# Performance work log

Measured on AMD Instinct MI355X. Metric: run time of the kernel, lower is better.

## Reference

```python
import jax, jax.numpy as jnp
import numpy as np
from jax import lax

# Production-scale RPN detection-head config
B, FH, FW, NA = 8, 200, 200, 9      # batch, fmap h, fmap w, anchors/cell
H, W = 800, 800                      # image dims
N = FH * FW * NA                     # 360k anchors per image
NMS_THR = 0.7
MIN_SIZE = 1e-3


def _make_anchors():
    scales = np.array([32.0, 64.0, 128.0])
    ratios = np.array([0.5, 1.0, 2.0])
    ws = (scales[:, None] * np.sqrt(1.0 / ratios)[None, :]).reshape(-1)  # [NA]
    hs = (scales[:, None] * np.sqrt(ratios)[None, :]).reshape(-1)
    sy, sx = H / FH, W / FW
    cx = (np.arange(FW) + 0.5) * sx
    cy = (np.arange(FH) + 0.5) * sy
    cxg, cyg = np.meshgrid(cx, cy)                     # [FH,FW]
    cxg = cxg[..., None]; cyg = cyg[..., None]         # [FH,FW,1]
    a = np.stack([cxg - ws / 2, cyg - hs / 2, cxg + ws / 2, cyg + hs / 2], axis=-1)
    return jnp.asarray(a.reshape(-1, 4), jnp.float32)  # [N,4] xyxy


def setup_inputs() -> dict:
    key = jax.random.key(0)
    k1, k2 = jax.random.split(key)
    cls_logits = jax.random.normal(k1, (B, N, 1), jnp.float32)
    reg_deltas = jax.random.normal(k2, (B, N, 4), jnp.float32) * 0.1  # sane exp(dw)
    anchors = jnp.broadcast_to(_make_anchors()[None], (B, N, 4))
    return {
        "cls_logits": cls_logits,
        "reg_deltas": reg_deltas,
        "anchors": anchors,
        "keep_pre_nms": 1000,
        "keep_post_nms": 300,
    }


def _offsets2boxes(deltas, anchors):
    aw = anchors[:, 2] - anchors[:, 0]
    ah = anchors[:, 3] - anchors[:, 1]
    acx = anchors[:, 0] + 0.5 * aw
    acy = anchors[:, 1] + 0.5 * ah
    cx = deltas[:, 0] * aw + acx
    cy = deltas[:, 1] * ah + acy
    w = jnp.exp(deltas[:, 2]) * aw
    h = jnp.exp(deltas[:, 3]) * ah
    return jnp.stack([cx - 0.5 * w, cy - 0.5 * h, cx + 0.5 * w, cy + 0.5 * h], axis=-1)


def _iou_matrix(b):
    area = (b[:, 2] - b[:, 0]) * (b[:, 3] - b[:, 1])
    lt = jnp.maximum(b[:, None, :2], b[None, :, :2])
    rb = jnp.minimum(b[:, None, 2:], b[None, :, 2:])
    wh = jnp.clip(rb - lt, 0.0)
    inter = wh[..., 0] * wh[..., 1]
    return inter / (area[:, None] + area[None, :] - inter + 1e-9)


def _detect_one(logit, delta, anc, pre, post):
    scores = jax.nn.sigmoid(logit.reshape(-1))             # [N]
    boxes = _offsets2boxes(delta.reshape(-1, 4), anc)      # [N,4]
    s, idx = lax.top_k(scores, pre)                        # sorted desc
    b = boxes[idx]                                         # [pre,4]
    # clip to image
    b = jnp.stack([
        jnp.clip(b[:, 0], 0.0, W), jnp.clip(b[:, 1], 0.0, H),
        jnp.clip(b[:, 2], 0.0, W), jnp.clip(b[:, 3], 0.0, H)], axis=-1)
    valid = ((b[:, 2] - b[:, 0]) >= MIN_SIZE) & ((b[:, 3] - b[:, 1]) >= MIN_SIZE)
    # greedy NMS on score-sorted boxes (mask-based, fixed shapes)
    iou = _iou_matrix(lax.stop_gradient(b))                # [pre,pre]
    j = jnp.arange(pre)

    def body(keep, i):
        sup = (iou[i] > NMS_THR) & (j > i) & keep[i]
        return keep & ~sup, None

    keep, _ = lax.scan(body, valid, jnp.arange(pre))
    # compact first `post` kept detections into fixed [post,5], zero-padded
    dets = jnp.concatenate([b, s[:, None]], axis=-1)       # [pre,5]
    rank = jnp.cumsum(keep) - 1
    tgt = jnp.where(keep & (rank < post), rank, post)
    out = jnp.zeros((post + 1, 5), dets.dtype).at[tgt].set(dets)[:post]
    return out


def reference(cls_logits, reg_deltas, anchors, keep_pre_nms, keep_post_nms):
    f = lambda l, d, a: _detect_one(l, d, a, keep_pre_nms, keep_post_nms)
    return jax.vmap(f)(cls_logits, reg_deltas, anchors)    # [B,post,5]
```

## Files before the change

### kernel.cpp

```cpp
#include <hip/hip_runtime.h>
#include <stdint.h>
#include <math.h>

typedef unsigned long long u64;
typedef unsigned int u32;
typedef unsigned short u16;

#define NPI   360000
#define B_IMG 8
#define PRE   1000
#define POST  300
#define CAP   4096
#define NMSF  0.7f
#define IMG_W 800.0f
#define IMG_H 800.0f

#define NBIN    4096
#define KSHIFT  20
#define CHUNK_H 24
#define F4PB_H  (NPI / 4 / CHUNK_H)
#define CHUNK_C 48
#define F4PB_C  (NPI / 4 / CHUNK_C)
#define EPB_C   (NPI / CHUNK_C)
#define LBUF    1024

#define CNT_OFF    0
#define VALID_OFF  128
#define THRESH_OFF 2048
#define RHIST_OFF  4096
#define BHIST_OFF  135168
#define CAND_OFF   1708032
#define BOX_OFF    1970176
#define SCORE_OFF  2098176
#define MASK_OFF   2130176

__device__ __forceinline__ u32 fkey(float f) {
  u32 u = __float_as_uint(f);
  return (u & 0x80000000u) ? ~u : (u | 0x80000000u);
}
__device__ __forceinline__ u64 rl64(u64 v, int lane) {
  u32 lo = (u32)__builtin_amdgcn_readlane((int)(u32)v, lane);
  u32 hi = (u32)__builtin_amdgcn_readlane((int)(u32)(v >> 32), lane);
  return ((u64)hi << 32) | lo;
}
__device__ __forceinline__ u64 sx64(u64 v, int m) {
  u32 lo = (u32)__shfl_xor((int)(u32)v, m, 64);
  u32 hi = (u32)__shfl_xor((int)(u32)(v >> 32), m, 64);
  return ((u64)hi << 32) | lo;
}

__global__ __launch_bounds__(256) void k_hist(const float* __restrict__ logits,
                                              u32* __restrict__ bhist) {
  __shared__ u32 h[NBIN];
  const int img = blockIdx.y, c = blockIdx.x;
  for (int i = threadIdx.x; i < NBIN; i += 256) h[i] = 0;
  __syncthreads();
  const float4* L = (const float4*)(logits + (size_t)img * NPI) + (size_t)c * F4PB_H;
  for (int i = threadIdx.x; i < F4PB_H; i += 256) {
    float4 v = L[i];
    atomicAdd(&h[fkey(v.x) >> KSHIFT], 1u);
    atomicAdd(&h[fkey(v.y) >> KSHIFT], 1u);
    atomicAdd(&h[fkey(v.z) >> KSHIFT], 1u);
    atomicAdd(&h[fkey(v.w) >> KSHIFT], 1u);
  }
  __syncthreads();
  u32* O = bhist + (size_t)(img * CHUNK_H + c) * (NBIN / 2);
  for (int i = threadIdx.x; i < NBIN / 2; i += 256)
    O[i] = (h[2 * i] & 0xFFFFu) | (h[2 * i + 1] << 16);
}

__global__ __launch_bounds__(256) void k_hreduce(const u32* __restrict__ bhist,
                                                 u32* __restrict__ rhist,
                                                 u32* __restrict__ cnt,
                                                 u64* __restrict__ validw) {
  int gid = blockIdx.x * 256 + threadIdx.x;
  int img = gid >> 11, p = gid & 2047;
  u32 slo = 0, shi = 0;
#pragma unroll
  for (int c = 0; c < CHUNK_H; c++) {
    u32 v = bhist[(size_t)(img * CHUNK_H + c) * (NBIN / 2) + p];
    slo += v & 0xFFFFu;
    shi += v >> 16;
  }
  ((uint2*)rhist)[img * (NBIN / 2) + p] = make_uint2(slo, shi);
  if (blockIdx.x == 0) {
    if (threadIdx.x < 8) cnt[threadIdx.x] = 0;
    if (threadIdx.x < 128) validw[threadIdx.x] = 0ull;
  }
}

__global__ void k_select(const u32* __restrict__ hist, int* __restrict__ thresh) {
  const int img = blockIdx.x;
  const u32* H = hist + img * NBIN;
  __shared__ u32 part[256];
  u32 s = 0;
#pragma unroll
  for (int b = 0; b < 16; b++) s += H[threadIdx.x * 16 + b];
  part[threadIdx.x] = s;
  __syncthreads();
  if (threadIdx.x == 0) {
    u32 cum = 0;
    int pb = 255;
    for (; pb > 0; pb--) {
      if (cum + part[pb] >= (u32)PRE) break;
      cum += part[pb];
    }
    int bin;
    for (bin = pb * 16 + 15; bin >= pb * 16; bin--) {
      cum += H[bin];
      if (cum >= (u32)PRE) break;
    }
    if (bin < pb * 16) bin = pb * 16;
    thresh[img] = bin;
  }
}

__global__ __launch_bounds__(256) void k_compact(const float* __restrict__ logits,
                                                 const int* __restrict__ thresh,
                                                 u32* __restrict__ cnt,
                                                 u64* __restrict__ cand) {
  __shared__ u64 buf[LBUF];
  __shared__ u32 bcnt;
  __shared__ u32 gbase;
  const int img = blockIdx.y, c = blockIdx.x;
  const int tb  = thresh[img];
  if (threadIdx.x == 0) bcnt = 0;
  __syncthreads();
  const float4* L = (const float4*)(logits + (size_t)img * NPI) + (size_t)c * F4PB_C;
  const int ebase = c * EPB_C;
  for (int i = threadIdx.x; i < F4PB_C; i += 256) {
    float4 v = L[i];
    float xs[4] = {v.x, v.y, v.z, v.w};
#pragma unroll
    for (int q = 0; q < 4; q++) {
      float x = xs[q];
      if ((int)(fkey(x) >> KSHIFT) >= tb) {
        float ef = (float)exp(-(double)x);
        float sg = 1.0f / (1.0f + ef);
        u32 e = (u32)(ebase + 4 * i + q);
        u32 p = atomicAdd(&bcnt, 1u);
        if (p < LBUF)
          buf[p] = ((u64)fkey(sg) << 32) | (u64)(0xFFFFFFFFu - e);
      }
    }
  }
  __syncthreads();
  if (threadIdx.x == 0) {
    u32 m = bcnt < LBUF ? bcnt : LBUF;
    bcnt = m;
    gbase = atomicAdd(&cnt[img], m);
  }
  __syncthreads();
  const u32 m = bcnt, gb = gbase;
  for (u32 j = threadIdx.x; j < m; j += 256) {
    u32 pos = gb + j;
    if (pos < CAP) cand[img * CAP + pos] = buf[j];
  }
}

#define RB 8
__device__ __forceinline__ void emit_row(
    int img, int row, u64 key,
    const float* __restrict__ deltas, const float* __restrict__ anchors,
    float4* __restrict__ boxes, float* __restrict__ scores, u64* __restrict__ validw) {
  u32 hi  = (u32)(key >> 32);
  u32 idx = 0xFFFFFFFFu - (u32)(key & 0xFFFFFFFFu);
  u32 su  = (hi & 0x80000000u) ? (hi ^ 0x80000000u) : ~hi;
  float sc = __uint_as_float(su);
  size_t off = (size_t)img * NPI + idx;
  float4 d = ((const float4*)deltas)[off];
  float4 a = ((const float4*)anchors)[off];
  float aw = a.z - a.x, ah = a.w - a.y;
  float acx = a.x + 0.5f * aw, acy = a.y + 0.5f * ah;
  float cx = d.x * aw + acx, cy = d.y * ah + acy;
  float w = expf(d.z) * aw, h = expf(d.w) * ah;
  float x1 = cx - 0.5f * w, y1 = cy - 0.5f * h;
  float x2 = cx + 0.5f * w, y2 = cy + 0.5f * h;
  x1 = fminf(fmaxf(x1, 0.f), IMG_W);
  y1 = fminf(fmaxf(y1, 0.f), IMG_H);
  x2 = fminf(fmaxf(x2, 0.f), IMG_W);
  y2 = fminf(fmaxf(y2, 0.f), IMG_H);
  boxes[img * PRE + row]  = make_float4(x1, y1, x2, y2);
  scores[img * PRE + row] = sc;
  if (((x2 - x1) >= 1e-3f) && ((y2 - y1) >= 1e-3f))
    atomicOr(&validw[img * 16 + (row >> 6)], 1ull << (row & 63));
}

__global__ __launch_bounds__(256) void k_rank(
    const float* __restrict__ deltas, const float* __restrict__ anchors,
    const u32* __restrict__ cnt, const u64* __restrict__ cand,
    float4* __restrict__ boxes, float* __restrict__ scores, u64* __restrict__ validw) {
  __shared__ u64 skey[CAP];
  const int img = blockIdx.y;
  int n = (int)cnt[img];
  if (n > CAP) n = CAP;
  for (int i = threadIdx.x; i < n; i += 256) skey[i] = cand[img * CAP + i];
  __syncthreads();
  const int r0 = blockIdx.x * 256 + threadIdx.x;
  const int r1 = r0 + RB * 256;
  u64 k0 = (r0 < n) ? skey[r0] : 0ull;
  u64 k1 = (r1 < n) ? skey[r1] : 0ull;
  int c0 = 0, c1 = 0;
  for (int j = 0; j < n; j++) {
    u64 kj = skey[j];
    c0 += (kj > k0);
    c1 += (kj > k1);
  }
  if (r0 < n && c0 < PRE) emit_row(img, c0, k0, deltas, anchors, boxes, scores, validw);
  if (r1 < n && c1 < PRE) emit_row(img, c1, k1, deltas, anchors, boxes, scores, validw);
}

__global__ __launch_bounds__(1024) void k_iou(const float4* __restrict__ boxes,
                                              u64* __restrict__ mask) {
  __shared__ float4 sb[1024];
  __shared__ float  sa[1024];
  const int img = blockIdx.y;
  const int tid = threadIdx.x;
  {
    float4 b = (tid < PRE) ? boxes[img * PRE + tid]
                           : make_float4(0.f, 0.f, 0.f, 0.f);
    sb[tid] = b;
    sa[tid] = (b.z - b.x) * (b.w - b.y);
  }
  __syncthreads();
  const int lane = tid & 63;
  const int wv   = tid >> 6;
  const int i    = blockIdx.x * 64 + lane;
  const bool rowok = (i < PRE);
  const float4 bi = sb[blockIdx.x * 64 + lane];
  const float  ai = sa[blockIdx.x * 64 + lane];
  const int cbase = wv << 6;
  u64 bits = 0;
#pragma unroll
  for (int k = 0; k < 64; k++) {
    int c = cbase + k;
    float4 bc = sb[c];
    float ac  = sa[c];
    float ltx = fmaxf(bi.x, bc.x), lty = fmaxf(bi.y, bc.y);
    float rbx = fminf(bi.z, bc.z), rby = fminf(bi.w, bc.w);
    float iw = fmaxf(rbx - ltx, 0.f), ih = fmaxf(rby - lty, 0.f);
    float inter = iw * ih;
    float iou = inter / (ai + ac - inter + 1e-9f);
    bits |= (iou > NMSF) ? (1ull << k) : 0ull;
  }
  int d = i - cbase;
  u64 gtmask = (d < 0) ? ~0ull : ((d >= 63) ? 0ull : (~0ull << (d + 1)));
  int rem = PRE - cbase;
  u64 tmask = (rem >= 64) ? ~0ull : ((rem <= 0) ? 0ull : ((1ull << rem) - 1ull));
  bits &= gtmask & tmask;
  if (rowok) mask[((size_t)img * PRE + i) * 16 + wv] = bits;
}

#define LDSROWS 496
#define NMS_T   320
__global__ __launch_bounds__(NMS_T) void k_nms(
    const u64* __restrict__ mask, const u64* __restrict__ validw,
    const float4* __restrict__ boxes, const float* __restrict__ scores,
    float* __restrict__ out) {
  __shared__ u64 smask[LDSROWS * 16];
  __shared__ int skeeplist[POST];
  __shared__ int skept;
  const int img = blockIdx.x;
  const int tid = threadIdx.x;
  const u64* M = mask + (size_t)img * PRE * 16;
  u64 diag[16];
  if (tid < 64) {
#pragma unroll
    for (int cc = 0; cc < 16; cc++) {
      int row = cc * 64 + tid;
      diag[cc] = (row < PRE) ? M[(size_t)row * 16 + cc] : 0ull;
    }
  }
  for (int e = tid; e < LDSROWS * 16; e += NMS_T) smask[e] = M[e];
  __syncthreads();
  if (tid < 64) {
    const int lane = tid;
    const int w = lane & 15, g = lane >> 4;
    u64 rem = ~0ull;
    if (lane < 16) {
      rem = ~validw[img * 16 + lane];
      if (lane == 15) rem |= 0xFFFFFF0000000000ull;
    }
    int kept = 0;
#pragma unroll
    for (int cc = 0; cc < 16; cc++) {
      u64 alive = ~rl64(rem, cc);
      int kept0 = kept;
      while (alive != 0ull && kept < POST) {
        int r = __builtin_ctzll(alive);
        if (lane == 0) skeeplist[kept] = cc * 64 + r;
        kept++;
        u64 sup = rl64(diag[cc], r);
        alive &= ~sup;
        alive &= ~(1ull << r);
      }
      int nc = kept - kept0;
      if (nc > 0 && kept < POST && cc < 15) {
        u64 part = 0;
        for (int j = g; j < nc; j += 4) {
          int row = skeeplist[kept0 + j];
          part |= (row < LDSROWS) ? smask[row * 16 + w] : M[(size_t)row * 16 + w];
        }
        part |= sx64(part, 16);
        part |= sx64(part, 32);
        rem |= part;
      }
      if (kept >= POST) break;
    }
    if (lane == 0) skept = kept;
  }
  __syncthreads();
  if (tid < POST) {
    float4 bx = make_float4(0.f, 0.f, 0.f, 0.f);
    float  sc = 0.f;
    if (tid < skept) {
      int i = skeeplist[tid];
      bx = boxes[img * PRE + i];
      sc = scores[img * PRE + i];
    }
    float* o = out + ((size_t)img * POST + tid) * 5;
    o[0] = bx.x; o[1] = bx.y; o[2] = bx.z; o[3] = bx.w; o[4] = sc;
  }
}

extern "C" void kernel_launch(void* const* d_in, const int* in_sizes, int n_in,
                              void* d_out, int out_size, void* d_ws, size_t ws_size,
                              hipStream_t stream) {
  const float* logits  = (const float*)d_in[0];
  const float* deltas  = (const float*)d_in[1];
  const float* anchors = (const float*)d_in[2];
  float* out = (float*)d_out;
  char* ws = (char*)d_ws;

  u32* cnt      = (u32*)(ws + CNT_OFF);
  u64* validw   = (u64*)(ws + VALID_OFF);
  int* thresh   = (int*)(ws + THRESH_OFF);
  u32* rhist    = (u32*)(ws + RHIST_OFF);
  u32* bhist    = (u32*)(ws + BHIST_OFF);
  u64* cand     = (u64*)(ws + CAND_OFF);
  float4* boxes = (float4*)(ws + BOX_OFF);
  float* scores = (float*)(ws + SCORE_OFF);
  u64* mask     = (u64*)(ws + MASK_OFF);

  dim3 gh(CHUNK_H, B_IMG);
  k_hist<<<gh, 256, 0, stream>>>(logits, bhist);
  k_hreduce<<<(B_IMG * NBIN / 2) / 256, 256, 0, stream>>>(bhist, rhist, cnt, validw);
  k_select<<<B_IMG, 256, 0, stream>>>(rhist, thresh);
  dim3 gc(CHUNK_C, B_IMG);
  k_compact<<<gc, 256, 0, stream>>>(logits, thresh, cnt, cand);
  dim3 gr(RB, B_IMG);
  k_rank<<<gr, 256, 0, stream>>>(deltas, anchors, cnt, cand, boxes, scores, validw);
  dim3 g2(16, B_IMG);
  k_iou<<<g2, 1024, 0, stream>>>(boxes, mask);
  k_nms<<<B_IMG, NMS_T, 0, stream>>>(mask, validw, boxes, scores, out);
}
```

Measured before the change: 214.2 us.

## Fuse rank, IoU and NMS into one per-image kernel; merge threshold select

Replaces the separate rank, IoU-mask and NMS kernels with a single 1024-thread block per image. Boxes, areas, scores and the valid bits stay in shared memory instead of round-tripping through global workspace. The histogram reduce and threshold-select kernels become one kernel that uses a wave-level suffix scan, and the histogram moves to 8192 bins over 36 chunks. This removes several launches and intermediate global traffic, but the rank and IoU work now runs on only 8 blocks instead of many. The NMS mask reads also lose their shared-memory staging and go to global memory.

```diff
diff --git a/kernel.cpp b/kernel.cpp
--- a/kernel.cpp
+++ b/kernel.cpp
@@ -4,7 +4,6 @@
 
 typedef unsigned long long u64;
 typedef unsigned int u32;
-typedef unsigned short u16;
 
 #define NPI   360000
 #define B_IMG 8
@@ -15,9 +14,9 @@
 #define IMG_W 800.0f
 #define IMG_H 800.0f
 
-#define NBIN    4096
-#define KSHIFT  20
-#define CHUNK_H 24
+#define NBIN    8192
+#define KSHIFT  19
+#define CHUNK_H 36
 #define F4PB_H  (NPI / 4 / CHUNK_H)
 #define CHUNK_C 48
 #define F4PB_C  (NPI / 4 / CHUNK_C)
@@ -25,14 +24,10 @@
 #define LBUF    1024
 
 #define CNT_OFF    0
-#define VALID_OFF  128
-#define THRESH_OFF 2048
-#define RHIST_OFF  4096
-#define BHIST_OFF  135168
-#define CAND_OFF   1708032
-#define BOX_OFF    1970176
-#define SCORE_OFF  2098176
-#define MASK_OFF   2130176
+#define THRESH_OFF 128
+#define BHIST_OFF  2048
+#define CAND_OFF   4720640
+#define MASK_OFF   4982784
 
 __device__ __forceinline__ u32 fkey(float f) {
   u32 u = __float_as_uint(f);
@@ -69,50 +64,49 @@
     O[i] = (h[2 * i] & 0xFFFFu) | (h[2 * i + 1] << 16);
 }
 
-__global__ __launch_bounds__(256) void k_hreduce(const u32* __restrict__ bhist,
-                                                 u32* __restrict__ rhist,
-                                                 u32* __restrict__ cnt,
-                                                 u64* __restrict__ validw) {
-  int gid = blockIdx.x * 256 + threadIdx.x;
-  int img = gid >> 11, p = gid & 2047;
-  u32 slo = 0, shi = 0;
-#pragma unroll
+__global__ __launch_bounds__(1024) void k_thresh(const u32* __restrict__ bhist,
+                                                 int* __restrict__ thresh,
+                                                 u32* __restrict__ cnt) {
+  const int img = blockIdx.x;
+  const int t = threadIdx.x;
+  const int lane = t & 63, w = t >> 6;
+  u32 binc[8];
+#pragma unroll
+  for (int b = 0; b < 8; b++) binc[b] = 0;
   for (int c = 0; c < CHUNK_H; c++) {
-    u32 v = bhist[(size_t)(img * CHUNK_H + c) * (NBIN / 2) + p];
-    slo += v & 0xFFFFu;
-    shi += v >> 16;
-  }
-  ((uint2*)rhist)[img * (NBIN / 2) + p] = make_uint2(slo, shi);
-  if (blockIdx.x == 0) {
-    if (threadIdx.x < 8) cnt[threadIdx.x] = 0;
-    if (threadIdx.x < 128) validw[threadIdx.x] = 0ull;
-  }
-}
-
-__global__ void k_select(const u32* __restrict__ hist, int* __restrict__ thresh) {
-  const int img = blockIdx.x;
-  const u32* H = hist + img * NBIN;
-  __shared__ u32 part[256];
+    uint4 v = ((const uint4*)(bhist + (size_t)(img * CHUNK_H + c) * (NBIN / 2)))[t];
+    binc[0] += v.x & 0xFFFFu; binc[1] += v.x >> 16;
+    binc[2] += v.y & 0xFFFFu; binc[3] += v.y >> 16;
+    binc[4] += v.z & 0xFFFFu; binc[5] += v.z >> 16;
+    binc[6] += v.w & 0xFFFFu; binc[7] += v.w >> 16;
+  }
   u32 s = 0;
 #pragma unroll
-  for (int b = 0; b < 16; b++) s += H[threadIdx.x * 16 + b];
-  part[threadIdx.x] = s;
-  __syncthreads();
-  if (threadIdx.x == 0) {
-    u32 cum = 0;
-    int pb = 255;
-    for (; pb > 0; pb--) {
-      if (cum + part[pb] >= (u32)PRE) break;
-      cum += part[pb];
-    }
-    int bin;
-    for (bin = pb * 16 + 15; bin >= pb * 16; bin--) {
-      cum += H[bin];
-      if (cum >= (u32)PRE) break;
-    }
-    if (bin < pb * 16) bin = pb * 16;
+  for (int b = 0; b < 8; b++) s += binc[b];
+  u32 suf = s;
+#pragma unroll
+  for (int off = 1; off < 64; off <<= 1) {
+    u32 o = (u32)__shfl_down((int)suf, off, 64);
+    if (lane + off < 64) suf += o;
+  }
+  __shared__ u32 wtot[16];
+  if (lane == 0) wtot[w] = suf;
+  __syncthreads();
+  u32 wsuf = 0;
+  for (int ww = w + 1; ww < 16; ww++) wsuf += wtot[ww];
+  u32 suffix_incl = suf + wsuf;
+  u32 s_excl = suffix_incl - s;
+  if (suffix_incl >= (u32)PRE && s_excl < (u32)PRE) {
+    u32 cum = s_excl;
+    int bin = 8 * t;
+#pragma unroll
+    for (int b = 7; b >= 0; b--) {
+      cum += binc[b];
+      if (cum >= (u32)PRE) { bin = 8 * t + b; break; }
+    }
     thresh[img] = bin;
   }
+  if (img == 0 && t < 8) cnt[t] = 0;
 }
 
 __global__ __launch_bounds__(256) void k_compact(const float* __restrict__ logits,
@@ -158,127 +152,121 @@
   }
 }
 
-#define RB 8
-__device__ __forceinline__ void emit_row(
-    int img, int row, u64 key,
-    const float* __restrict__ deltas, const float* __restrict__ anchors,
-    float4* __restrict__ boxes, float* __restrict__ scores, u64* __restrict__ validw) {
-  u32 hi  = (u32)(key >> 32);
-  u32 idx = 0xFFFFFFFFu - (u32)(key & 0xFFFFFFFFu);
-  u32 su  = (hi & 0x80000000u) ? (hi ^ 0x80000000u) : ~hi;
-  float sc = __uint_as_float(su);
-  size_t off = (size_t)img * NPI + idx;
-  float4 d = ((const float4*)deltas)[off];
-  float4 a = ((const float4*)anchors)[off];
-  float aw = a.z - a.x, ah = a.w - a.y;
-  float acx = a.x + 0.5f * aw, acy = a.y + 0.5f * ah;
-  float cx = d.x * aw + acx, cy = d.y * ah + acy;
-  float w = expf(d.z) * aw, h = expf(d.w) * ah;
-  float x1 = cx - 0.5f * w, y1 = cy - 0.5f * h;
-  float x2 = cx + 0.5f * w, y2 = cy + 0.5f * h;
-  x1 = fminf(fmaxf(x1, 0.f), IMG_W);
-  y1 = fminf(fmaxf(y1, 0.f), IMG_H);
-  x2 = fminf(fmaxf(x2, 0.f), IMG_W);
-  y2 = fminf(fmaxf(y2, 0.f), IMG_H);
-  boxes[img * PRE + row]  = make_float4(x1, y1, x2, y2);
-  scores[img * PRE + row] = sc;
-  if (((x2 - x1) >= 1e-3f) && ((y2 - y1) >= 1e-3f))
-    atomicOr(&validw[img * 16 + (row >> 6)], 1ull << (row & 63));
-}
-
-__global__ __launch_bounds__(256) void k_rank(
+__global__ __launch_bounds__(1024) void k_mega(
     const float* __restrict__ deltas, const float* __restrict__ anchors,
     const u32* __restrict__ cnt, const u64* __restrict__ cand,
-    float4* __restrict__ boxes, float* __restrict__ scores, u64* __restrict__ validw) {
+    u64* __restrict__ mask, float* __restrict__ out) {
   __shared__ u64 skey[CAP];
-  const int img = blockIdx.y;
-  int n = (int)cnt[img];
-  if (n > CAP) n = CAP;
-  for (int i = threadIdx.x; i < n; i += 256) skey[i] = cand[img * CAP + i];
-  __syncthreads();
-  const int r0 = blockIdx.x * 256 + threadIdx.x;
-  const int r1 = r0 + RB * 256;
-  u64 k0 = (r0 < n) ? skey[r0] : 0ull;
-  u64 k1 = (r1 < n) ? skey[r1] : 0ull;
-  int c0 = 0, c1 = 0;
-  for (int j = 0; j < n; j++) {
-    u64 kj = skey[j];
-    c0 += (kj > k0);
-    c1 += (kj > k1);
-  }
-  if (r0 < n && c0 < PRE) emit_row(img, c0, k0, deltas, anchors, boxes, scores, validw);
-  if (r1 < n && c1 < PRE) emit_row(img, c1, k1, deltas, anchors, boxes, scores, validw);
-}
-
-__global__ __launch_bounds__(1024) void k_iou(const float4* __restrict__ boxes,
-                                              u64* __restrict__ mask) {
-  __shared__ float4 sb[1024];
-  __shared__ float  sa[1024];
-  const int img = blockIdx.y;
-  const int tid = threadIdx.x;
-  {
-    float4 b = (tid < PRE) ? boxes[img * PRE + tid]
-                           : make_float4(0.f, 0.f, 0.f, 0.f);
-    sb[tid] = b;
-    sa[tid] = (b.z - b.x) * (b.w - b.y);
-  }
-  __syncthreads();
-  const int lane = tid & 63;
-  const int wv   = tid >> 6;
-  const int i    = blockIdx.x * 64 + lane;
-  const bool rowok = (i < PRE);
-  const float4 bi = sb[blockIdx.x * 64 + lane];
-  const float  ai = sa[blockIdx.x * 64 + lane];
-  const int cbase = wv << 6;
-  u64 bits = 0;
-#pragma unroll
-  for (int k = 0; k < 64; k++) {
-    int c = cbase + k;
-    float4 bc = sb[c];
-    float ac  = sa[c];
-    float ltx = fmaxf(bi.x, bc.x), lty = fmaxf(bi.y, bc.y);
-    float rbx = fminf(bi.z, bc.z), rby = fminf(bi.w, bc.w);
-    float iw = fmaxf(rbx - ltx, 0.f), ih = fmaxf(rby - lty, 0.f);
-    float inter = iw * ih;
-    float iou = inter / (ai + ac - inter + 1e-9f);
-    bits |= (iou > NMSF) ? (1ull << k) : 0ull;
-  }
-  int d = i - cbase;
-  u64 gtmask = (d < 0) ? ~0ull : ((d >= 63) ? 0ull : (~0ull << (d + 1)));
-  int rem = PRE - cbase;
-  u64 tmask = (rem >= 64) ? ~0ull : ((rem <= 0) ? 0ull : ((1ull << rem) - 1ull));
-  bits &= gtmask & tmask;
-  if (rowok) mask[((size_t)img * PRE + i) * 16 + wv] = bits;
-}
-
-#define LDSROWS 496
-#define NMS_T   320
-__global__ __launch_bounds__(NMS_T) void k_nms(
-    const u64* __restrict__ mask, const u64* __restrict__ validw,
-    const float4* __restrict__ boxes, const float* __restrict__ scores,
-    float* __restrict__ out) {
-  __shared__ u64 smask[LDSROWS * 16];
+  __shared__ float4 sbox[1024];
+  __shared__ float sarea[1024];
+  __shared__ float sscore[1024];
+  __shared__ u64 svalid[16];
   __shared__ int skeeplist[POST];
   __shared__ int skept;
   const int img = blockIdx.x;
   const int tid = threadIdx.x;
-  const u64* M = mask + (size_t)img * PRE * 16;
-  u64 diag[16];
-  if (tid < 64) {
-#pragma unroll
-    for (int cc = 0; cc < 16; cc++) {
-      int row = cc * 64 + tid;
-      diag[cc] = (row < PRE) ? M[(size_t)row * 16 + cc] : 0ull;
-    }
-  }
-  for (int e = tid; e < LDSROWS * 16; e += NMS_T) smask[e] = M[e];
-  __syncthreads();
+  u64* M = mask + (size_t)img * PRE * 16;
+
+  int n = (int)cnt[img];
+  if (n > CAP) n = CAP;
+  sbox[tid] = make_float4(0.f, 0.f, 0.f, 0.f);
+  sarea[tid] = 0.f; sscore[tid] = 0.f;
+  if (tid < 16) svalid[tid] = 0ull;
+#pragma unroll
+  for (int r = 0; r < CAP / 1024; r++) {
+    int i = tid + r * 1024;
+    skey[i] = (i < n) ? cand[img * CAP + i] : 0ull;
+  }
+  __syncthreads();
+
+  u64 kr[CAP / 1024];
+  int cr[CAP / 1024];
+#pragma unroll
+  for (int r = 0; r < CAP / 1024; r++) { kr[r] = skey[tid + r * 1024]; cr[r] = 0; }
+  const int nn = (n + 1) & ~1;
+  for (int j = 0; j < nn; j += 2) {
+    u64 kj0 = skey[j], kj1 = skey[j + 1];
+#pragma unroll
+    for (int r = 0; r < CAP / 1024; r++) {
+      cr[r] += (kj0 > kr[r]);
+      cr[r] += (kj1 > kr[r]);
+    }
+  }
+#pragma unroll
+  for (int r = 0; r < CAP / 1024; r++) {
+    int row = tid + r * 1024;
+    int rk = cr[r];
+    if (row < n && rk < PRE) {
+      u64 key = kr[r];
+      u32 hi  = (u32)(key >> 32);
+      u32 idx = 0xFFFFFFFFu - (u32)(key & 0xFFFFFFFFu);
+      u32 su  = (hi & 0x80000000u) ? (hi ^ 0x80000000u) : ~hi;
+      float sc = __uint_as_float(su);
+      size_t off = (size_t)img * NPI + idx;
+      float4 d = ((const float4*)deltas)[off];
+      float4 a = ((const float4*)anchors)[off];
+      float aw = a.z - a.x, ah = a.w - a.y;
+      float acx = a.x + 0.5f * aw, acy = a.y + 0.5f * ah;
+      float cx = d.x * aw + acx, cy = d.y * ah + acy;
+      float w = expf(d.z) * aw, h = expf(d.w) * ah;
+      float x1 = cx - 0.5f * w, y1 = cy - 0.5f * h;
+      float x2 = cx + 0.5f * w, y2 = cy + 0.5f * h;
+      x1 = fminf(fmaxf(x1, 0.f), IMG_W);
+      y1 = fminf(fmaxf(y1, 0.f), IMG_H);
+      x2 = fminf(fmaxf(x2, 0.f), IMG_W);
+      y2 = fminf(fmaxf(y2, 0.f), IMG_H);
+      sbox[rk]  = make_float4(x1, y1, x2, y2);
+      sarea[rk] = (x2 - x1) * (y2 - y1);
+      sscore[rk] = sc;
+      if (((x2 - x1) >= 1e-3f) && ((y2 - y1) >= 1e-3f))
+        atomicOr(&svalid[rk >> 6], 1ull << (rk & 63));
+    }
+  }
+  __syncthreads();
+
+  {
+    const int lane = tid & 63;
+    const int wv   = tid >> 6;
+    const int cbase = wv << 6;
+    int rem = PRE - cbase;
+    u64 tmask = (rem >= 64) ? ~0ull : ((rem <= 0) ? 0ull : ((1ull << rem) - 1ull));
+#pragma unroll
+    for (int rc = 0; rc < 16; rc++) {
+      int i = rc * 64 + lane;
+      float4 bi = sbox[i];
+      float  ai = sarea[i];
+      u64 bits = 0;
+#pragma unroll
+      for (int k = 0; k < 64; k++) {
+        float4 bc = sbox[cbase + k];
+        float ac  = sarea[cbase + k];
+        float ltx = fmaxf(bi.x, bc.x), lty = fmaxf(bi.y, bc.y);
+        float rbx = fminf(bi.z, bc.z), rby = fminf(bi.w, bc.w);
+        float iw = fmaxf(rbx - ltx, 0.f), ih = fmaxf(rby - lty, 0.f);
+        float inter = iw * ih;
+        float iou = inter / (ai + ac - inter + 1e-9f);
+        bits |= (iou > NMSF) ? (1ull << k) : 0ull;
+      }
+      int d = i - cbase;
+      u64 gtmask = (d < 0) ? ~0ull : ((d >= 63) ? 0ull : (~0ull << (d + 1)));
+      bits &= gtmask & tmask;
+      if (i < PRE) M[(size_t)i * 16 + wv] = bits;
+    }
+  }
+  __syncthreads();
+
   if (tid < 64) {
     const int lane = tid;
+    u64 diag[16];
+#pragma unroll
+    for (int cc = 0; cc < 16; cc++) {
+      int row = cc * 64 + lane;
+      diag[cc] = (row < PRE) ? M[(size_t)row * 16 + cc] : 0ull;
+    }
     const int w = lane & 15, g = lane >> 4;
     u64 rem = ~0ull;
     if (lane < 16) {
-      rem = ~validw[img * 16 + lane];
+      rem = ~svalid[lane];
       if (lane == 15) rem |= 0xFFFFFF0000000000ull;
     }
     int kept = 0;
@@ -299,7 +287,7 @@
         u64 part = 0;
         for (int j = g; j < nc; j += 4) {
           int row = skeeplist[kept0 + j];
-          part |= (row < LDSROWS) ? smask[row * 16 + w] : M[(size_t)row * 16 + w];
+          part |= M[(size_t)row * 16 + w];
         }
         part |= sx64(part, 16);
         part |= sx64(part, 32);
@@ -310,13 +298,14 @@
     if (lane == 0) skept = kept;
   }
   __syncthreads();
+
   if (tid < POST) {
     float4 bx = make_float4(0.f, 0.f, 0.f, 0.f);
     float  sc = 0.f;
     if (tid < skept) {
       int i = skeeplist[tid];
-      bx = boxes[img * PRE + i];
-      sc = scores[img * PRE + i];
+      bx = sbox[i];
+      sc = sscore[i];
     }
     float* o = out + ((size_t)img * POST + tid) * 5;
     o[0] = bx.x; o[1] = bx.y; o[2] = bx.z; o[3] = bx.w; o[4] = sc;
@@ -332,25 +321,16 @@
   float* out = (float*)d_out;
   char* ws = (char*)d_ws;
 
-  u32* cnt      = (u32*)(ws + CNT_OFF);
-  u64* validw   = (u64*)(ws + VALID_OFF);
-  int* thresh   = (int*)(ws + THRESH_OFF);
-  u32* rhist    = (u32*)(ws + RHIST_OFF);
-  u32* bhist    = (u32*)(ws + BHIST_OFF);
-  u64* cand     = (u64*)(ws + CAND_OFF);
-  float4* boxes = (float4*)(ws + BOX_OFF);
-  float* scores = (float*)(ws + SCORE_OFF);
-  u64* mask     = (u64*)(ws + MASK_OFF);
+  u32* cnt    = (u32*)(ws + CNT_OFF);
+  int* thresh = (int*)(ws + THRESH_OFF);
+  u32* bhist  = (u32*)(ws + BHIST_OFF);
+  u64* cand   = (u64*)(ws + CAND_OFF);
+  u64* mask   = (u64*)(ws + MASK_OFF);
 
   dim3 gh(CHUNK_H, B_IMG);
   k_hist<<<gh, 256, 0, stream>>>(logits, bhist);
-  k_hreduce<<<(B_IMG * NBIN / 2) / 256, 256, 0, stream>>>(bhist, rhist, cnt, validw);
-  k_select<<<B_IMG, 256, 0, stream>>>(rhist, thresh);
+  k_thresh<<<B_IMG, 1024, 0, stream>>>(bhist, thresh, cnt);
   dim3 gc(CHUNK_C, B_IMG);
   k_compact<<<gc, 256, 0, stream>>>(logits, thresh, cnt, cand);
-  dim3 gr(RB, B_IMG);
-  k_rank<<<gr, 256, 0, stream>>>(deltas, anchors, cnt, cand, boxes, scores, validw);
-  dim3 g2(16, B_IMG);
-  k_iou<<<g2, 1024, 0, stream>>>(boxes, mask);
-  k_nms<<<B_IMG, NMS_T, 0, stream>>>(mask, validw, boxes, scores, out);
-}
+  k_mega<<<B_IMG, 1024, 0, stream>>>(deltas, anchors, cnt, cand, mask, out);
+}
```

New measurement: 780.6 us. 264% more time.

## Fuse histogram reduce and threshold select into one kernel with finer bins

Applied to the files above, without the earlier changes.

Merges the histogram reduction and threshold-selection kernels into a single 1024-thread-per-image kernel that sums per-chunk histograms and finds the top-PRE bin with a wave-level suffix scan. This removes one launch and the round trip through a reduced-histogram buffer. It also doubles the bin count (shift 19) and raises the number of histogram chunks, so fewer candidates fall into the threshold bin and the compaction step has less work. In exchange the histogram kernel uses twice as much shared memory and writes a larger per-chunk histogram buffer, and the workspace layout is reshuffled.

```diff
diff --git a/kernel.cpp b/kernel.cpp
--- a/kernel.cpp
+++ b/kernel.cpp
@@ -4,7 +4,6 @@
 
 typedef unsigned long long u64;
 typedef unsigned int u32;
-typedef unsigned short u16;
 
 #define NPI   360000
 #define B_IMG 8
@@ -15,9 +14,9 @@
 #define IMG_W 800.0f
 #define IMG_H 800.0f
 
-#define NBIN    4096
-#define KSHIFT  20
-#define CHUNK_H 24
+#define NBIN    8192
+#define KSHIFT  19
+#define CHUNK_H 36
 #define F4PB_H  (NPI / 4 / CHUNK_H)
 #define CHUNK_C 48
 #define F4PB_C  (NPI / 4 / CHUNK_C)
@@ -25,14 +24,13 @@
 #define LBUF    1024
 
 #define CNT_OFF    0
-#define VALID_OFF  128
-#define THRESH_OFF 2048
-#define RHIST_OFF  4096
-#define BHIST_OFF  135168
-#define CAND_OFF   1708032
-#define BOX_OFF    1970176
-#define SCORE_OFF  2098176
-#define MASK_OFF   2130176
+#define THRESH_OFF 128
+#define VALID_OFF  256
+#define BOX_OFF    2048
+#define SCORE_OFF  130048
+#define BHIST_OFF  163840
+#define CAND_OFF   4882432
+#define MASK_OFF   5144576
 
 __device__ __forceinline__ u32 fkey(float f) {
   u32 u = __float_as_uint(f);
@@ -69,49 +67,52 @@
     O[i] = (h[2 * i] & 0xFFFFu) | (h[2 * i + 1] << 16);
 }
 
-__global__ __launch_bounds__(256) void k_hreduce(const u32* __restrict__ bhist,
-                                                 u32* __restrict__ rhist,
+__global__ __launch_bounds__(1024) void k_thresh(const u32* __restrict__ bhist,
+                                                 int* __restrict__ thresh,
                                                  u32* __restrict__ cnt,
                                                  u64* __restrict__ validw) {
-  int gid = blockIdx.x * 256 + threadIdx.x;
-  int img = gid >> 11, p = gid & 2047;
-  u32 slo = 0, shi = 0;
-#pragma unroll
+  const int img = blockIdx.x;
+  const int t = threadIdx.x;
+  const int lane = t & 63, w = t >> 6;
+  u32 binc[8];
+#pragma unroll
+  for (int b = 0; b < 8; b++) binc[b] = 0;
   for (int c = 0; c < CHUNK_H; c++) {
-    u32 v = bhist[(size_t)(img * CHUNK_H + c) * (NBIN / 2) + p];
-    slo += v & 0xFFFFu;
-    shi += v >> 16;
-  }
-  ((uint2*)rhist)[img * (NBIN / 2) + p] = make_uint2(slo, shi);
-  if (blockIdx.x == 0) {
-    if (threadIdx.x < 8) cnt[threadIdx.x] = 0;
-    if (threadIdx.x < 128) validw[threadIdx.x] = 0ull;
-  }
-}
-
-__global__ void k_select(const u32* __restrict__ hist, int* __restrict__ thresh) {
-  const int img = blockIdx.x;
-  const u32* H = hist + img * NBIN;
-  __shared__ u32 part[256];
+    uint4 v = ((const uint4*)(bhist + (size_t)(img * CHUNK_H + c) * (NBIN / 2)))[t];
+    binc[0] += v.x & 0xFFFFu; binc[1] += v.x >> 16;
+    binc[2] += v.y & 0xFFFFu; binc[3] += v.y >> 16;
+    binc[4] += v.z & 0xFFFFu; binc[5] += v.z >> 16;
+    binc[6] += v.w & 0xFFFFu; binc[7] += v.w >> 16;
+  }
   u32 s = 0;
 #pragma unroll
-  for (int b = 0; b < 16; b++) s += H[threadIdx.x * 16 + b];
-  part[threadIdx.x] = s;
-  __syncthreads();
-  if (threadIdx.x == 0) {
-    u32 cum = 0;
-    int pb = 255;
-    for (; pb > 0; pb--) {
-      if (cum + part[pb] >= (u32)PRE) break;
-      cum += part[pb];
-    }
-    int bin;
-    for (bin = pb * 16 + 15; bin >= pb * 16; bin--) {
-      cum += H[bin];
-      if (cum >= (u32)PRE) break;
-    }
-    if (bin < pb * 16) bin = pb * 16;
+  for (int b = 0; b < 8; b++) s += binc[b];
+  u32 suf = s;
+#pragma unroll
+  for (int off = 1; off < 64; off <<= 1) {
+    u32 o = (u32)__shfl_down((int)suf, off, 64);
+    if (lane + off < 64) suf += o;
+  }
+  __shared__ u32 wtot[16];
+  if (lane == 0) wtot[w] = suf;
+  __syncthreads();
+  u32 wsuf = 0;
+  for (int ww = w + 1; ww < 16; ww++) wsuf += wtot[ww];
+  u32 suffix_incl = suf + wsuf;
+  u32 s_excl = suffix_incl - s;
+  if (suffix_incl >= (u32)PRE && s_excl < (u32)PRE) {
+    u32 cum = s_excl;
+    int bin = 8 * t;
+#pragma unroll
+    for (int b = 7; b >= 0; b--) {
+      cum += binc[b];
+      if (cum >= (u32)PRE) { bin = 8 * t + b; break; }
+    }
     thresh[img] = bin;
+  }
+  if (img == 0) {
+    if (t < 8) cnt[t] = 0;
+    if (t < 128) validw[t] = 0ull;
   }
 }
 
@@ -333,19 +334,17 @@
   char* ws = (char*)d_ws;
 
   u32* cnt      = (u32*)(ws + CNT_OFF);
+  int* thresh   = (int*)(ws + THRESH_OFF);
   u64* validw   = (u64*)(ws + VALID_OFF);
-  int* thresh   = (int*)(ws + THRESH_OFF);
-  u32* rhist    = (u32*)(ws + RHIST_OFF);
+  float4* boxes = (float4*)(ws + BOX_OFF);
+  float* scores = (float*)(ws + SCORE_OFF);
   u32* bhist    = (u32*)(ws + BHIST_OFF);
   u64* cand     = (u64*)(ws + CAND_OFF);
-  float4* boxes = (float4*)(ws + BOX_OFF);
-  float* scores = (float*)(ws + SCORE_OFF);
   u64* mask     = (u64*)(ws + MASK_OFF);
 
   dim3 gh(CHUNK_H, B_IMG);
   k_hist<<<gh, 256, 0, stream>>>(logits, bhist);
-  k_hreduce<<<(B_IMG * NBIN / 2) / 256, 256, 0, stream>>>(bhist, rhist, cnt, validw);
-  k_select<<<B_IMG, 256, 0, stream>>>(rhist, thresh);
+  k_thresh<<<B_IMG, 1024, 0, stream>>>(bhist, thresh, cnt, validw);
   dim3 gc(CHUNK_C, B_IMG);
   k_compact<<<gc, 256, 0, stream>>>(logits, thresh, cnt, cand);
   dim3 gr(RB, B_IMG);
```

New measurement: 212.4 us. No clear change (-0.8%).
